# Optimization experiments

Hardware: AMD Instinct MI355X
Metric: run time of the kernel (lower is better)

Reference implementation:

```python
import jax, jax.numpy as jnp
import numpy as np

COMMITMENT_COST = 0.25
KLD_SCALE = 1.0


def setup_inputs() -> dict:
    key = jax.random.key(0)
    k1, k2 = jax.random.split(key)
    z = jax.random.normal(k1, (8, 4096, 512), dtype=jnp.float32)
    embed_w = jax.random.normal(k2, (1024, 512), dtype=jnp.float32)
    return {"z": z, "embed_w": embed_w}


def reference(z, embed_w):
    bsz, s, d = z.shape
    flat = z.reshape(-1, d)  # [N, d]
    dist = (
        jnp.sum(flat * flat, axis=1, keepdims=True)
        - 2.0 * flat @ embed_w.T
        + jnp.sum(embed_w * embed_w, axis=1)[None, :]
    )
    ind = jnp.argmin(dist, axis=1).reshape(bsz, s)  # (-dist).max == dist.min
    z_q = embed_w[ind]  # codebook gather [bsz, s, d]
    sg = jax.lax.stop_gradient
    diff = COMMITMENT_COST * ((sg(z_q) - z) ** 2 + (z_q - sg(z)) ** 2)
    diff = diff * KLD_SCALE
    z_q = z + sg(z_q - z)  # straight-through estimator
    return z_q, diff, ind
```

## Files before the change

### kernel.cpp

```cpp
#include <hip/hip_runtime.h>
#include <math.h>


#define D_DIM   512
#define K_CODES 1024
#define N_TOK   32768

#define BM   128
#define BN   128
#define BKP  32
#define NKT  (D_DIM / BKP)
#define LDSB 144

typedef __attribute__((ext_vector_type(8))) short bf16x8;
typedef __attribute__((ext_vector_type(4))) float f32x4;

__device__ __forceinline__ unsigned short bf16_rne(float f) {
    unsigned int u = __float_as_uint(f);
    return (unsigned short)((u + 0x7FFFu + ((u >> 16) & 1u)) >> 16);
}
__device__ __forceinline__ float bf16_to_f32(unsigned short b) {
    return __uint_as_float(((unsigned int)b) << 16);
}

__global__ __launch_bounds__(256) void vq_prep(const float* __restrict__ ew,
                                               unsigned short* __restrict__ ehi,
                                               unsigned short* __restrict__ elo,
                                               float* __restrict__ e2) {
    const int wv = threadIdx.x >> 6, lane = threadIdx.x & 63;
    const int code = blockIdx.x * 4 + wv;
    const float* row = ew + (size_t)code * D_DIM;
    float s = 0.0f;
#pragma unroll
    for (int h = 0; h < 2; ++h) {
        const int c = h * 256 + lane * 4;
        float4 v = *(const float4*)(row + c);
        float f[4] = {v.x, v.y, v.z, v.w};
        unsigned short hb[4], lb[4];
#pragma unroll
        for (int j = 0; j < 4; ++j) {
            s = fmaf(f[j], f[j], s);
            hb[j] = bf16_rne(f[j]);
            lb[j] = bf16_rne(f[j] - bf16_to_f32(hb[j]));
        }
        *(ushort4*)(ehi + (size_t)code * D_DIM + c) = make_ushort4(hb[0], hb[1], hb[2], hb[3]);
        *(ushort4*)(elo + (size_t)code * D_DIM + c) = make_ushort4(lb[0], lb[1], lb[2], lb[3]);
    }
#pragma unroll
    for (int off = 32; off > 0; off >>= 1) s += __shfl_xor(s, off, 64);
    if (lane == 0) e2[code] = s;
}

__global__ __launch_bounds__(256, 2) void vq_gemm(
    const float* __restrict__ z, const unsigned short* __restrict__ ehi,
    const unsigned short* __restrict__ elo, const float* __restrict__ e2,
    float* __restrict__ pv, float* __restrict__ pif) {
    __shared__ __align__(16) char lds[(BM + BN) * LDSB];
    char* As = lds;
    char* Bs = lds + BM * LDSB;

    const int t = threadIdx.x;
    const int bid = blockIdx.x;
    const int ntile = bid >> 8;
    const int mtile = bid & 255;
    const int row0 = mtile * BM;
    const int c0g  = ntile * BN;

    const int ar = t >> 3;
    const int ac = t & 7;
    const int bc  = t >> 1;
    const int bq0 = (t & 1) * 2;

    const int wv = t >> 6, lane = t & 63;
    const int wr = wv >> 1, wc = wv & 1;
    const int lm = lane & 15, lk = lane >> 4;

    f32x4 acc[4][4];
    const f32x4 zero4 = {0.f, 0.f, 0.f, 0.f};
#pragma unroll
    for (int i = 0; i < 4; ++i)
#pragma unroll
        for (int j = 0; j < 4; ++j) acc[i][j] = zero4;

    float4 aReg[4];
    uint4  bhReg[2], blReg[2];

    auto stage_load = [&](int kt) {
        const int k0 = kt * BKP;
#pragma unroll
        for (int p = 0; p < 4; ++p)
            aReg[p] = *(const float4*)(z + (size_t)(row0 + ar + 32 * p) * D_DIM + k0 + ac * 4);
#pragma unroll
        for (int q = 0; q < 2; ++q) {
            const int ch = bq0 + q;
            bhReg[q] = *(const uint4*)(ehi + (size_t)(c0g + bc) * D_DIM + k0 + ch * 8);
            blReg[q] = *(const uint4*)(elo + (size_t)(c0g + bc) * D_DIM + k0 + ch * 8);
        }
    };
    auto stage_write = [&]() {
#pragma unroll
        for (int p = 0; p < 4; ++p) {
            char* rowp = As + (ar + 32 * p) * LDSB;
            float f[4] = {aReg[p].x, aReg[p].y, aReg[p].z, aReg[p].w};
            unsigned short hb[4], lb[4];
#pragma unroll
            for (int j = 0; j < 4; ++j) {
                hb[j] = bf16_rne(f[j]);
                lb[j] = bf16_rne(f[j] - bf16_to_f32(hb[j]));
            }
            *(ushort4*)(rowp + ac * 8)      = make_ushort4(hb[0], hb[1], hb[2], hb[3]);
            *(ushort4*)(rowp + 64 + ac * 8) = make_ushort4(lb[0], lb[1], lb[2], lb[3]);
        }
#pragma unroll
        for (int q = 0; q < 2; ++q) {
            const int ch = bq0 + q;
            char* rowp = Bs + bc * LDSB;
            *(uint4*)(rowp + ch * 16)      = bhReg[q];
            *(uint4*)(rowp + 64 + ch * 16) = blReg[q];
        }
    };
    auto compute = [&]() {
        const int sA[3] = {0, 0, 64};
        const int sB[3] = {0, 64, 0};
#pragma unroll
        for (int s = 0; s < 3; ++s) {
            bf16x8 af[4], bfr[4];
#pragma unroll
            for (int mi = 0; mi < 4; ++mi) {
                const int r = wr * 64 + mi * 16 + lm;
                af[mi] = *(const bf16x8*)(As + r * LDSB + sA[s] + lk * 16);
            }
#pragma unroll
            for (int nj = 0; nj < 4; ++nj) {
                const int c = wc * 64 + nj * 16 + lm;
                bfr[nj] = *(const bf16x8*)(Bs + c * LDSB + sB[s] + lk * 16);
            }
#pragma unroll
            for (int mi = 0; mi < 4; ++mi)
#pragma unroll
                for (int nj = 0; nj < 4; ++nj)
                    acc[mi][nj] = __builtin_amdgcn_mfma_f32_16x16x32_bf16(
                        af[mi], bfr[nj], acc[mi][nj], 0, 0, 0);
        }
    };

    stage_load(0);
    stage_write();
    for (int kt = 0; kt < NKT; ++kt) {
        __syncthreads();
        if (kt + 1 < NKT) stage_load(kt + 1);
        compute();
        __syncthreads();
        if (kt + 1 < NKT) stage_write();
    }

    float best[16], bidx[16];
#pragma unroll
    for (int i = 0; i < 16; ++i) { best[i] = INFINITY; bidx[i] = 0.f; }
#pragma unroll
    for (int nj = 0; nj < 4; ++nj) {
        const int cloc = wc * 64 + nj * 16 + lm;
        const float e2v = e2[c0g + cloc];
#pragma unroll
        for (int mi = 0; mi < 4; ++mi)
#pragma unroll
            for (int r = 0; r < 4; ++r) {
                const float sc = fmaf(-2.0f, acc[mi][nj][r], e2v);
                const int bi = mi * 4 + r;
                if (sc < best[bi]) { best[bi] = sc; bidx[bi] = (float)(c0g + cloc); }
            }
    }
#pragma unroll
    for (int off = 1; off < 16; off <<= 1) {
#pragma unroll
        for (int bi = 0; bi < 16; ++bi) {
            float v2 = __shfl_xor(best[bi], off, 64);
            float i2 = __shfl_xor(bidx[bi], off, 64);
            if (v2 < best[bi] || (v2 == best[bi] && i2 < bidx[bi])) {
                best[bi] = v2; bidx[bi] = i2;
            }
        }
    }
    __syncthreads();
    float* sv = (float*)lds;
    float* si = sv + 256;
    if (lm == 0) {
#pragma unroll
        for (int mi = 0; mi < 4; ++mi)
#pragma unroll
            for (int r = 0; r < 4; ++r) {
                const int rl = wr * 64 + mi * 16 + lk * 4 + r;
                sv[wc * 128 + rl] = best[mi * 4 + r];
                si[wc * 128 + rl] = bidx[mi * 4 + r];
            }
    }
    __syncthreads();
    if (t < 128) {
        float v0 = sv[t], i0 = si[t];
        float v1 = sv[128 + t], i1 = si[128 + t];
        if (v1 < v0 || (v1 == v0 && i1 < i0)) { v0 = v1; i0 = i1; }
        pv [(size_t)ntile * N_TOK + row0 + t] = v0;
        pif[(size_t)ntile * N_TOK + row0 + t] = i0;
    }
}

__global__ __launch_bounds__(256) void vq_reduce(const float* __restrict__ pv,
                                                 const float* __restrict__ pif,
                                                 float* __restrict__ indf) {
    const int row = blockIdx.x * 256 + threadIdx.x;
    float v = pv[row], ix = pif[row];
#pragma unroll
    for (int nb = 1; nb < 8; ++nb) {
        float v2 = pv[(size_t)nb * N_TOK + row];
        float i2 = pif[(size_t)nb * N_TOK + row];
        if (v2 < v || (v2 == v && i2 < ix)) { v = v2; ix = i2; }
    }
    indf[row] = ix;
}

__global__ __launch_bounds__(256) void vq_out_kernel(
    const float* __restrict__ z, const float* __restrict__ ew,
    const float* __restrict__ indf, float* __restrict__ zq,
    float* __restrict__ diff) {
    const int w    = threadIdx.x >> 6;
    const int lane = threadIdx.x & 63;
    const int row  = blockIdx.x * 4 + w;
    const int c    = (int)indf[row];

    const float4* z4 = (const float4*)&z[(size_t)row * D_DIM];
    const float4* e4 = (const float4*)&ew[(size_t)c * D_DIM];
    float4* q4 = (float4*)&zq[(size_t)row * D_DIM];
    float4* d4 = (float4*)&diff[(size_t)row * D_DIM];

#pragma unroll
    for (int v = 0; v < 2; ++v) {
        const int i = v * 64 + lane;
        const float4 zv = z4[i];
        const float4 ev = e4[i];
        float4 qv, dv;
        float ax = ev.x - zv.x, ay = ev.y - zv.y, az = ev.z - zv.z, aw = ev.w - zv.w;
        qv.x = zv.x + ax; qv.y = zv.y + ay; qv.z = zv.z + az; qv.w = zv.w + aw;
        dv.x = 0.5f * (ax * ax); dv.y = 0.5f * (ay * ay);
        dv.z = 0.5f * (az * az); dv.w = 0.5f * (aw * aw);
        q4[i] = qv;
        d4[i] = dv;
    }
}

extern "C" void kernel_launch(void* const* d_in, const int* in_sizes, int n_in,
                              void* d_out, int out_size, void* d_ws, size_t ws_size,
                              hipStream_t stream) {
    const float* z  = (const float*)d_in[0];
    const float* ew = (const float*)d_in[1];
    float* out  = (float*)d_out;
    float* zq   = out;
    float* diff = out + (size_t)N_TOK * D_DIM;
    float* indf = out + (size_t)2 * N_TOK * D_DIM;

    char* scratch = (char*)d_out;
    unsigned short* ehi = (unsigned short*)(scratch);
    unsigned short* elo = (unsigned short*)(scratch + (1u << 20));
    float* e2  = (float*)(scratch + (2u << 20));
    float* pv  = (float*)(scratch + (2u << 20) + 4096);
    float* pif = (float*)(scratch + (3u << 20) + 4096);

    hipLaunchKernelGGL(vq_prep,   dim3(K_CODES / 4), dim3(256), 0, stream, ew, ehi, elo, e2);
    hipLaunchKernelGGL(vq_gemm,   dim3(2048),        dim3(256), 0, stream, z, ehi, elo, e2, pv, pif);
    hipLaunchKernelGGL(vq_reduce, dim3(N_TOK / 256), dim3(256), 0, stream, pv, pif, indf);
    hipLaunchKernelGGL(vq_out_kernel, dim3(N_TOK / 4), dim3(256), 0, stream, z, ew, indf, zq, diff);
}
```

Measured before the change: 237.3 us.

## Pre-split z into bf16 hi/lo and stream GEMM tiles via global_load_lds

Adds a separate kernel that converts z into bf16 hi and lo arrays in a scratch area of the output buffer, so the GEMM no longer converts inside its main loop. The GEMM now loads tiles straight from global memory into LDS with global_load_lds, uses a k-major LDS layout without padding, swizzles the block-to-tile mapping, and raises the occupancy hint to 3. The register prefetch double-buffering is gone, so each k-step issues its loads and then waits at a barrier. The extra pass writes and rereads about 64MB of bf16 data, and the unpadded layout may cause LDS bank conflicts.

```diff
diff --git a/kernel.cpp b/kernel.cpp
--- a/kernel.cpp
+++ b/kernel.cpp
@@ -6,11 +6,9 @@
 #define K_CODES 1024
 #define N_TOK   32768
 
-#define BM   128
-#define BN   128
-#define BKP  32
-#define NKT  (D_DIM / BKP)
-#define LDSB 144
+#define BM 128
+#define BN 128
+#define NKT 16
 
 typedef __attribute__((ext_vector_type(8))) short bf16x8;
 typedef __attribute__((ext_vector_type(4))) float f32x4;
@@ -21,6 +19,34 @@
 }
 __device__ __forceinline__ float bf16_to_f32(unsigned short b) {
     return __uint_as_float(((unsigned int)b) << 16);
+}
+
+#define GLOAD16(gp, lp)                                                        \
+    __builtin_amdgcn_global_load_lds(                                          \
+        (const __attribute__((address_space(1))) void*)(gp),                   \
+        (__attribute__((address_space(3))) void*)(lp), 16, 0, 0)
+
+__global__ __launch_bounds__(256) void vq_zsplit(const float* __restrict__ z,
+                                                 unsigned short* __restrict__ zhi,
+                                                 unsigned short* __restrict__ zlo) {
+    const int tid = blockIdx.x * 256 + threadIdx.x;
+    const float4* z4 = (const float4*)z;
+    ushort4* h4 = (ushort4*)zhi;
+    ushort4* l4 = (ushort4*)zlo;
+#pragma unroll
+    for (int g = 0; g < 8; ++g) {
+        const size_t i = (size_t)g * 524288 + tid;
+        float4 v = z4[i];
+        float f[4] = {v.x, v.y, v.z, v.w};
+        unsigned short hb[4], lb[4];
+#pragma unroll
+        for (int j = 0; j < 4; ++j) {
+            hb[j] = bf16_rne(f[j]);
+            lb[j] = bf16_rne(f[j] - bf16_to_f32(hb[j]));
+        }
+        h4[i] = make_ushort4(hb[0], hb[1], hb[2], hb[3]);
+        l4[i] = make_ushort4(lb[0], lb[1], lb[2], lb[3]);
+    }
 }
 
 __global__ __launch_bounds__(256) void vq_prep(const float* __restrict__ ew,
@@ -51,27 +77,31 @@
     if (lane == 0) e2[code] = s;
 }
 
-__global__ __launch_bounds__(256, 2) void vq_gemm(
-    const float* __restrict__ z, const unsigned short* __restrict__ ehi,
-    const unsigned short* __restrict__ elo, const float* __restrict__ e2,
-    float* __restrict__ pv, float* __restrict__ pif) {
-    __shared__ __align__(16) char lds[(BM + BN) * LDSB];
-    char* As = lds;
-    char* Bs = lds + BM * LDSB;
-
-    const int t = threadIdx.x;
-    const int bid = blockIdx.x;
-    const int ntile = bid >> 8;
-    const int mtile = bid & 255;
+__global__ __launch_bounds__(256, 3) void vq_gemm(
+    const unsigned short* __restrict__ zhi, const unsigned short* __restrict__ zlo,
+    const unsigned short* __restrict__ ehi, const unsigned short* __restrict__ elo,
+    const float* __restrict__ e2, float* __restrict__ pv, float* __restrict__ pif) {
+    __shared__ __align__(16) unsigned short lds[16384];
+    const int AHI = 0, ALO = 4096, BHI = 8192, BLO = 12288;
+
+    const int t = threadIdx.x, lane = t & 63, wv = t >> 6;
+    const int b  = blockIdx.x;
+    const int wg = (b & 7) * 256 + (b >> 3);
+    const int mtile = wg >> 3, ntile = wg & 7;
     const int row0 = mtile * BM;
     const int c0g  = ntile * BN;
 
-    const int ar = t >> 3;
-    const int ac = t & 7;
-    const int bc  = t >> 1;
-    const int bq0 = (t & 1) * 2;
-
-    const int wv = t >> 6, lane = t & 63;
+    const int idx0 = (wv * 2 + 0) * 64 + lane;
+    const int idx1 = (wv * 2 + 1) * 64 + lane;
+    const int c_0 = idx0 >> 7, r_0 = idx0 & 127;
+    const int c_1 = idx1 >> 7, r_1 = idx1 & 127;
+    const size_t zo0 = (size_t)(row0 + r_0) * D_DIM + c_0 * 8;
+    const size_t zo1 = (size_t)(row0 + r_1) * D_DIM + c_1 * 8;
+    const size_t eo0 = (size_t)(c0g + r_0) * D_DIM + c_0 * 8;
+    const size_t eo1 = (size_t)(c0g + r_1) * D_DIM + c_1 * 8;
+    const int l0 = (wv * 2 + 0) * 512;
+    const int l1 = (wv * 2 + 1) * 512;
+
     const int wr = wv >> 1, wc = wv & 1;
     const int lm = lane & 15, lk = lane >> 4;
 
@@ -82,76 +112,50 @@
 #pragma unroll
         for (int j = 0; j < 4; ++j) acc[i][j] = zero4;
 
-    float4 aReg[4];
-    uint4  bhReg[2], blReg[2];
-
-    auto stage_load = [&](int kt) {
-        const int k0 = kt * BKP;
-#pragma unroll
-        for (int p = 0; p < 4; ++p)
-            aReg[p] = *(const float4*)(z + (size_t)(row0 + ar + 32 * p) * D_DIM + k0 + ac * 4);
-#pragma unroll
-        for (int q = 0; q < 2; ++q) {
-            const int ch = bq0 + q;
-            bhReg[q] = *(const uint4*)(ehi + (size_t)(c0g + bc) * D_DIM + k0 + ch * 8);
-            blReg[q] = *(const uint4*)(elo + (size_t)(c0g + bc) * D_DIM + k0 + ch * 8);
-        }
-    };
-    auto stage_write = [&]() {
-#pragma unroll
-        for (int p = 0; p < 4; ++p) {
-            char* rowp = As + (ar + 32 * p) * LDSB;
-            float f[4] = {aReg[p].x, aReg[p].y, aReg[p].z, aReg[p].w};
-            unsigned short hb[4], lb[4];
-#pragma unroll
-            for (int j = 0; j < 4; ++j) {
-                hb[j] = bf16_rne(f[j]);
-                lb[j] = bf16_rne(f[j] - bf16_to_f32(hb[j]));
-            }
-            *(ushort4*)(rowp + ac * 8)      = make_ushort4(hb[0], hb[1], hb[2], hb[3]);
-            *(ushort4*)(rowp + 64 + ac * 8) = make_ushort4(lb[0], lb[1], lb[2], lb[3]);
-        }
-#pragma unroll
-        for (int q = 0; q < 2; ++q) {
-            const int ch = bq0 + q;
-            char* rowp = Bs + bc * LDSB;
-            *(uint4*)(rowp + ch * 16)      = bhReg[q];
-            *(uint4*)(rowp + 64 + ch * 16) = blReg[q];
-        }
-    };
-    auto compute = [&]() {
-        const int sA[3] = {0, 0, 64};
-        const int sB[3] = {0, 64, 0};
-#pragma unroll
-        for (int s = 0; s < 3; ++s) {
-            bf16x8 af[4], bfr[4];
-#pragma unroll
-            for (int mi = 0; mi < 4; ++mi) {
-                const int r = wr * 64 + mi * 16 + lm;
-                af[mi] = *(const bf16x8*)(As + r * LDSB + sA[s] + lk * 16);
-            }
-#pragma unroll
-            for (int nj = 0; nj < 4; ++nj) {
-                const int c = wc * 64 + nj * 16 + lm;
-                bfr[nj] = *(const bf16x8*)(Bs + c * LDSB + sB[s] + lk * 16);
-            }
-#pragma unroll
-            for (int mi = 0; mi < 4; ++mi)
-#pragma unroll
-                for (int nj = 0; nj < 4; ++nj)
-                    acc[mi][nj] = __builtin_amdgcn_mfma_f32_16x16x32_bf16(
-                        af[mi], bfr[nj], acc[mi][nj], 0, 0, 0);
-        }
-    };
-
-    stage_load(0);
-    stage_write();
     for (int kt = 0; kt < NKT; ++kt) {
+        const int ko = kt * 32;
+        GLOAD16(zhi + zo0 + ko, &lds[AHI + l0]);
+        GLOAD16(zhi + zo1 + ko, &lds[AHI + l1]);
+        GLOAD16(zlo + zo0 + ko, &lds[ALO + l0]);
+        GLOAD16(zlo + zo1 + ko, &lds[ALO + l1]);
+        GLOAD16(ehi + eo0 + ko, &lds[BHI + l0]);
+        GLOAD16(ehi + eo1 + ko, &lds[BHI + l1]);
+        GLOAD16(elo + eo0 + ko, &lds[BLO + l0]);
+        GLOAD16(elo + eo1 + ko, &lds[BLO + l1]);
         __syncthreads();
-        if (kt + 1 < NKT) stage_load(kt + 1);
-        compute();
+
+        bf16x8 ah[4], al[4], bh[4], bl[4];
+#pragma unroll
+        for (int mi = 0; mi < 4; ++mi) {
+            const int s = (lk * 128 + wr * 64 + mi * 16 + lm) * 8;
+            ah[mi] = *(const bf16x8*)&lds[AHI + s];
+            al[mi] = *(const bf16x8*)&lds[ALO + s];
+        }
+#pragma unroll
+        for (int nj = 0; nj < 4; ++nj) {
+            const int s = (lk * 128 + wc * 64 + nj * 16 + lm) * 8;
+            bh[nj] = *(const bf16x8*)&lds[BHI + s];
+            bl[nj] = *(const bf16x8*)&lds[BLO + s];
+        }
+#pragma unroll
+        for (int mi = 0; mi < 4; ++mi)
+#pragma unroll
+            for (int nj = 0; nj < 4; ++nj)
+                acc[mi][nj] = __builtin_amdgcn_mfma_f32_16x16x32_bf16(
+                    ah[mi], bh[nj], acc[mi][nj], 0, 0, 0);
+#pragma unroll
+        for (int mi = 0; mi < 4; ++mi)
+#pragma unroll
+            for (int nj = 0; nj < 4; ++nj)
+                acc[mi][nj] = __builtin_amdgcn_mfma_f32_16x16x32_bf16(
+                    ah[mi], bl[nj], acc[mi][nj], 0, 0, 0);
+#pragma unroll
+        for (int mi = 0; mi < 4; ++mi)
+#pragma unroll
+            for (int nj = 0; nj < 4; ++nj)
+                acc[mi][nj] = __builtin_amdgcn_mfma_f32_16x16x32_bf16(
+                    al[mi], bh[nj], acc[mi][nj], 0, 0, 0);
         __syncthreads();
-        if (kt + 1 < NKT) stage_write();
     }
 
     float best[16], bidx[16];
@@ -257,15 +261,20 @@
     float* diff = out + (size_t)N_TOK * D_DIM;
     float* indf = out + (size_t)2 * N_TOK * D_DIM;
 
-    char* scratch = (char*)d_out;
-    unsigned short* ehi = (unsigned short*)(scratch);
-    unsigned short* elo = (unsigned short*)(scratch + (1u << 20));
-    float* e2  = (float*)(scratch + (2u << 20));
-    float* pv  = (float*)(scratch + (2u << 20) + 4096);
-    float* pif = (float*)(scratch + (3u << 20) + 4096);
-
+    char* s0 = (char*)d_out;
+    unsigned short* ehi = (unsigned short*)(s0);
+    unsigned short* elo = (unsigned short*)(s0 + (1u << 20));
+    float* e2  = (float*)(s0 + (2u << 20));
+    float* pv  = (float*)(s0 + (2u << 20) + 4096);
+    float* pif = (float*)(s0 + (3u << 20) + 4096);
+    unsigned short* zhi = (unsigned short*)diff;
+    unsigned short* zlo = zhi + (size_t)N_TOK * D_DIM;
+
+    hipLaunchKernelGGL(vq_zsplit, dim3(2048),       dim3(256), 0, stream, z, zhi, zlo);
     hipLaunchKernelGGL(vq_prep,   dim3(K_CODES / 4), dim3(256), 0, stream, ew, ehi, elo, e2);
-    hipLaunchKernelGGL(vq_gemm,   dim3(2048),        dim3(256), 0, stream, z, ehi, elo, e2, pv, pif);
+    hipLaunchKernelGGL(vq_gemm,   dim3(2048),       dim3(256), 0, stream,
+                       zhi, zlo, ehi, elo, e2, pv, pif);
     hipLaunchKernelGGL(vq_reduce, dim3(N_TOK / 256), dim3(256), 0, stream, pv, pif, indf);
-    hipLaunchKernelGGL(vq_out_kernel, dim3(N_TOK / 4), dim3(256), 0, stream, z, ew, indf, zq, diff);
-}
+    hipLaunchKernelGGL(vq_out_kernel, dim3(N_TOK / 4), dim3(256), 0, stream,
+                       z, ew, indf, zq, diff);
+}
```

Result: faster. 196.9 us (-17.0%).
